# Performance work log

Hardware: AMD Instinct MI355X
Metric: run time of the kernel (lower is better)

Reference implementation:

```python
import jax, jax.numpy as jnp
import numpy as np

B, N, D = 8, 512, 768
HS = 64          # gp_head_size
NT = 12          # len(tag_vocab)
NEG = 1e12


def setup_inputs() -> dict:
    key = jax.random.key(0)
    ks = jax.random.split(key, 14)
    s = 0.02  # init scale for weights
    return {
        "chars": jax.random.normal(ks[0], (B, N, D), dtype=jnp.float32),
        "mask": jax.random.randint(ks[1], (B, N), 0, 2).astype(jnp.int32),
        "w1_ent": jax.random.normal(ks[2], (2 * HS, D), dtype=jnp.float32) * s,
        "b1_ent": jax.random.normal(ks[3], (2 * HS,), dtype=jnp.float32) * s,
        "w2_ent": jax.random.normal(ks[4], (2 * 2, 2 * HS), dtype=jnp.float32) * s,
        "b2_ent": jax.random.normal(ks[5], (2 * 2,), dtype=jnp.float32) * s,
        "w1_head": jax.random.normal(ks[6], (2 * HS, D), dtype=jnp.float32) * s,
        "b1_head": jax.random.normal(ks[7], (2 * HS,), dtype=jnp.float32) * s,
        "w2_head": jax.random.normal(ks[8], (2 * NT, 2 * HS), dtype=jnp.float32) * s,
        "b2_head": jax.random.normal(ks[9], (2 * NT,), dtype=jnp.float32) * s,
        "w1_tail": jax.random.normal(ks[10], (2 * HS, D), dtype=jnp.float32) * s,
        "b1_tail": jax.random.normal(ks[11], (2 * HS,), dtype=jnp.float32) * s,
        "w2_tail": jax.random.normal(ks[12], (2 * NT, 2 * HS), dtype=jnp.float32) * s,
        "b2_tail": jax.random.normal(ks[13], (2 * NT,), dtype=jnp.float32) * s,
    }


def _egp(x, w1, b1, w2, b2, mask, head_size, rope, tril):
    # x: [B,N,D] -> h: [B,N,2*head_size]
    h = jnp.einsum('bnd,ed->bne', x, w1) + b1
    qw, kw = h[..., 0::2], h[..., 1::2]          # [B,N,head_size] each
    if rope:
        n = x.shape[1]
        pos = jnp.arange(n, dtype=x.dtype)
        inv = jnp.power(10000.0, -2.0 * jnp.arange(head_size // 2, dtype=x.dtype) / head_size)
        ang = pos[:, None] * inv[None, :]         # [N, head_size/2]
        cos = jnp.repeat(jnp.cos(ang), 2, axis=-1)[None]  # [1,N,head_size]
        sin = jnp.repeat(jnp.sin(ang), 2, axis=-1)[None]
        def rot(t):
            t2 = jnp.stack([-t[..., 1::2], t[..., 0::2]], axis=-1).reshape(t.shape)
            return t * cos + t2 * sin
        qw, kw = rot(qw), rot(kw)
    logits = jnp.einsum('bmd,bnd->bmn', qw, kw) / (head_size ** 0.5)  # [B,M,N]
    bias = (jnp.einsum('bne,he->bnh', h, w2) + b2).transpose(0, 2, 1) / 2.0  # [B,2H,N]
    # [B,H,M,N]
    logits = logits[:, None] + bias[:, 0::2, None, :] + bias[:, 1::2, :, None]
    m = mask.astype(logits.dtype)
    pad = 1.0 - m[:, None, None, :] * m[:, None, :, None]
    logits = logits - pad * NEG
    if tril:
        tri = jnp.tril(jnp.ones((logits.shape[-2], logits.shape[-1]), logits.dtype), k=-1)
        logits = logits - tri * NEG
    return logits


def reference(chars, mask, w1_ent, b1_ent, w2_ent, b2_ent,
              w1_head, b1_head, w2_head, b2_head,
              w1_tail, b1_tail, w2_tail, b2_tail):
    entity = _egp(chars, w1_ent, b1_ent, w2_ent, b2_ent, mask, HS, True, True)
    head = _egp(chars, w1_head, b1_head, w2_head, b2_head, mask, HS, False, False)
    tail = _egp(chars, w1_tail, b1_tail, w2_tail, b2_tail, mask, HS, False, False)
    return (entity, head, tail)
```

## Files before the change

### kernel.cpp

```cpp
#include <hip/hip_runtime.h>
#include <cstddef>

namespace {
constexpr int B_ = 8;
constexpr int N_ = 512;
constexpr int D_ = 768;
constexpr int HS_ = 64;
constexpr int M_ = B_ * N_;
constexpr int E_ = 2 * HS_;
constexpr float NEGV = 1000000000000.0f;
constexpr float LOG2_10000 = 13.287712379549449f;
}

typedef short mfrag_t __attribute__((ext_vector_type(8)));
typedef float macc_t  __attribute__((ext_vector_type(4)));

__device__ __forceinline__ unsigned short bft(float x) {
    union { float f; unsigned u; } c; c.f = x;
    return (unsigned short)(c.u >> 16);
}

__global__ __launch_bounds__(256) void prep_kernel(
    const float* __restrict__ chars,
    const float* __restrict__ w1e, const float* __restrict__ b1e,
    const float* __restrict__ w2e, const float* __restrict__ b2e,
    const float* __restrict__ w1h, const float* __restrict__ b1h,
    const float* __restrict__ w2h, const float* __restrict__ b2h,
    const float* __restrict__ w1t, const float* __restrict__ b1t,
    const float* __restrict__ w2t, const float* __restrict__ b2t,
    float* __restrict__ h_base,
    float* __restrict__ bias_e, float* __restrict__ bias_h, float* __restrict__ bias_t)
{
    const int fam = blockIdx.y;
    const float* w1 = (fam == 0) ? w1e : (fam == 1) ? w1h : w1t;
    const float* b1 = (fam == 0) ? b1e : (fam == 1) ? b1h : b1t;
    const float* w2 = (fam == 0) ? w2e : (fam == 1) ? w2h : w2t;
    const float* b2 = (fam == 0) ? b2e : (fam == 1) ? b2h : b2t;
    float* bout = (fam == 0) ? bias_e : (fam == 1) ? bias_h : bias_t;
    const int H2 = (fam == 0) ? 4 : 24;
    float* hout = h_base + (size_t)fam * M_ * E_;
    const int m0 = blockIdx.x * 64;

    __shared__ unsigned short A_lds[64][40];
    __shared__ unsigned short B_lds[128][40];
    __shared__ float hs[64][132];

    const int t    = threadIdx.x;
    const int w    = t >> 6;
    const int lane = t & 63;
    const int ml   = lane & 15;
    const int quad = lane >> 4;

    const int ar = t >> 2;
    const int ak = (t & 3) * 8;
    const int bc = t >> 1;
    const int bk = (t & 1) * 16;

    const float* aptr = chars + (size_t)(m0 + ar) * D_ + ak;
    const float* bptr = w1 + (size_t)bc * D_ + bk;

    macc_t acc[8];
    #pragma unroll
    for (int f = 0; f < 8; ++f) acc[f] = (macc_t)0.0f;

    float4 av0 = *(const float4*)(aptr);
    float4 av1 = *(const float4*)(aptr + 4);
    float4 bv0 = *(const float4*)(bptr);
    float4 bv1 = *(const float4*)(bptr + 4);
    float4 bv2 = *(const float4*)(bptr + 8);
    float4 bv3 = *(const float4*)(bptr + 12);

    for (int s = 0; s < 24; ++s) {
        {
            mfrag_t pa;
            pa[0] = (short)bft(av0.x); pa[1] = (short)bft(av0.y);
            pa[2] = (short)bft(av0.z); pa[3] = (short)bft(av0.w);
            pa[4] = (short)bft(av1.x); pa[5] = (short)bft(av1.y);
            pa[6] = (short)bft(av1.z); pa[7] = (short)bft(av1.w);
            *(mfrag_t*)&A_lds[ar][ak] = pa;
            mfrag_t pb0, pb1;
            pb0[0] = (short)bft(bv0.x); pb0[1] = (short)bft(bv0.y);
            pb0[2] = (short)bft(bv0.z); pb0[3] = (short)bft(bv0.w);
            pb0[4] = (short)bft(bv1.x); pb0[5] = (short)bft(bv1.y);
            pb0[6] = (short)bft(bv1.z); pb0[7] = (short)bft(bv1.w);
            pb1[0] = (short)bft(bv2.x); pb1[1] = (short)bft(bv2.y);
            pb1[2] = (short)bft(bv2.z); pb1[3] = (short)bft(bv2.w);
            pb1[4] = (short)bft(bv3.x); pb1[5] = (short)bft(bv3.y);
            pb1[6] = (short)bft(bv3.z); pb1[7] = (short)bft(bv3.w);
            *(mfrag_t*)&B_lds[bc][bk]     = pb0;
            *(mfrag_t*)&B_lds[bc][bk + 8] = pb1;
        }
        __syncthreads();
        if (s < 23) {
            aptr += 32; bptr += 32;
            av0 = *(const float4*)(aptr);
            av1 = *(const float4*)(aptr + 4);
            bv0 = *(const float4*)(bptr);
            bv1 = *(const float4*)(bptr + 4);
            bv2 = *(const float4*)(bptr + 8);
            bv3 = *(const float4*)(bptr + 12);
        }
        const mfrag_t afrag = *(const mfrag_t*)&A_lds[w * 16 + ml][quad * 8];
        #pragma unroll
        for (int f = 0; f < 8; ++f) {
            const mfrag_t bfrag = *(const mfrag_t*)&B_lds[f * 16 + ml][quad * 8];
            acc[f] = __builtin_amdgcn_mfma_f32_16x16x32_bf16(afrag, bfrag, acc[f], 0, 0, 0);
        }
        __syncthreads();
    }

    #pragma unroll
    for (int f = 0; f < 8; ++f) {
        const int col = f * 16 + ml;
        const float bb1 = b1[col];
        #pragma unroll
        for (int r = 0; r < 4; ++r)
            hs[w * 16 + quad * 4 + r][col] = acc[f][r] + bb1;
    }
    __syncthreads();

    {
        const int row = t >> 2;
        const int c0  = (t & 3) * 32;
        float* hp = hout + (size_t)(m0 + row) * E_ + c0;
        #pragma unroll
        for (int q = 0; q < 8; ++q)
            *(float4*)(hp + 4 * q) = *(const float4*)&hs[row][c0 + 4 * q];
    }

    {
        const int row = t & 63;
        const int h2b = t >> 6;
        const int P   = H2 >> 2;
        const int bb  = m0 >> 9;
        const int nb  = (m0 & 511) + row;
        float accv[6] = {0, 0, 0, 0, 0, 0};
        for (int e0 = 0; e0 < E_; e0 += 16) {
            float4 hv0 = *(const float4*)&hs[row][e0];
            float4 hv1 = *(const float4*)&hs[row][e0 + 4];
            float4 hv2 = *(const float4*)&hs[row][e0 + 8];
            float4 hv3 = *(const float4*)&hs[row][e0 + 12];
            for (int p = 0; p < P; ++p) {
                const float* wr = w2 + (size_t)(h2b + 4 * p) * E_ + e0;
                const float4 w0 = *(const float4*)(wr);
                const float4 w1v = *(const float4*)(wr + 4);
                const float4 w2v = *(const float4*)(wr + 8);
                const float4 w3v = *(const float4*)(wr + 12);
                accv[p] += hv0.x * w0.x + hv0.y * w0.y + hv0.z * w0.z + hv0.w * w0.w
                         + hv1.x * w1v.x + hv1.y * w1v.y + hv1.z * w1v.z + hv1.w * w1v.w
                         + hv2.x * w2v.x + hv2.y * w2v.y + hv2.z * w2v.z + hv2.w * w2v.w
                         + hv3.x * w3v.x + hv3.y * w3v.y + hv3.z * w3v.z + hv3.w * w3v.w;
            }
        }
        for (int p = 0; p < P; ++p) {
            const int h2 = h2b + 4 * p;
            bout[((size_t)bb * H2 + h2) * N_ + nb] = (accv[p] + b2[h2]) * 0.5f;
        }
    }
}

template <int H, bool ROPE, bool TRIL>
__device__ __forceinline__ void egp_tile(
    const float* __restrict__ hfam, const float* __restrict__ biasfam,
    const int* __restrict__ mask, float* __restrict__ out,
    int b, int m0, int n0, float (*qtT)[68], float (*kt)[68], int t)
{
    const int srow = t >> 2;
    const int sch  = t & 3;

    {
        const float* hq = hfam + (size_t)(b * N_ + m0 + srow) * E_;
        const float* hk = hfam + (size_t)(b * N_ + n0 + srow) * E_;
        #pragma unroll
        for (int jj = 0; jj < 8; ++jj) {
            const int i = sch + 4 * jj;
            const float4 v = *(const float4*)(hq + 4 * i);
            const float4 w = *(const float4*)(hk + 4 * i);
            if (ROPE) {
                const float inv = exp2f(-(float)i * (LOG2_10000 / 32.0f));
                float sq, cq, sk, ck;
                sincosf((float)(m0 + srow) * inv, &sq, &cq);
                sincosf((float)(n0 + srow) * inv, &sk, &ck);
                qtT[2 * i + 0][srow] = v.x * cq - v.z * sq;
                qtT[2 * i + 1][srow] = v.z * cq + v.x * sq;
                kt [2 * i + 0][srow] = w.y * ck - w.w * sk;
                kt [2 * i + 1][srow] = w.w * ck + w.y * sk;
            } else {
                qtT[2 * i + 0][srow] = v.x;
                qtT[2 * i + 1][srow] = v.z;
                kt [2 * i + 0][srow] = w.y;
                kt [2 * i + 1][srow] = w.w;
            }
        }
    }
    __syncthreads();

    const int rq = t >> 4;
    const int cq = t & 15;

    float acc[4][4] = {};
    #pragma unroll 8
    for (int k = 0; k < 64; ++k) {
        const float4 av = *(const float4*)&qtT[k][4 * rq];
        const float4 kv = *(const float4*)&kt [k][4 * cq];
        acc[0][0] += av.x * kv.x; acc[0][1] += av.x * kv.y; acc[0][2] += av.x * kv.z; acc[0][3] += av.x * kv.w;
        acc[1][0] += av.y * kv.x; acc[1][1] += av.y * kv.y; acc[1][2] += av.y * kv.z; acc[1][3] += av.y * kv.w;
        acc[2][0] += av.z * kv.x; acc[2][1] += av.z * kv.y; acc[2][2] += av.z * kv.z; acc[2][3] += av.z * kv.w;
        acc[3][0] += av.w * kv.x; acc[3][1] += av.w * kv.y; acc[3][2] += av.w * kv.z; acc[3][3] += av.w * kv.w;
    }

    #pragma unroll
    for (int j = 0; j < 4; ++j)
        #pragma unroll
        for (int q = 0; q < 4; ++q) acc[j][q] *= 0.125f;

    int mrow[4], mm[4];
    #pragma unroll
    for (int j = 0; j < 4; ++j) {
        mrow[j] = m0 + 4 * rq + j;
        mm[j]   = mask[b * N_ + mrow[j]];
    }
    const int ncol = n0 + 4 * cq;
    const int4 mnv = *(const int4*)(mask + b * N_ + ncol);
    const int mn[4] = { mnv.x, mnv.y, mnv.z, mnv.w };

    #pragma unroll
    for (int hh = 0; hh < H; ++hh) {
        const float4 be = *(const float4*)(biasfam + ((size_t)b * 2 * H + 2 * hh) * N_ + ncol);
        float bo[4];
        #pragma unroll
        for (int j = 0; j < 4; ++j)
            bo[j] = biasfam[((size_t)b * 2 * H + 2 * hh + 1) * N_ + mrow[j]];

        #pragma unroll
        for (int j = 0; j < 4; ++j) {
            float o[4] = { acc[j][0] + be.x + bo[j], acc[j][1] + be.y + bo[j],
                           acc[j][2] + be.z + bo[j], acc[j][3] + be.w + bo[j] };
            #pragma unroll
            for (int q = 0; q < 4; ++q) {
                if (!(mm[j] & mn[q])) o[q] -= NEGV;
                if (TRIL && (ncol + q) < mrow[j]) o[q] -= NEGV;
            }
            *(float4*)(out + ((size_t)(b * H + hh) * N_ + mrow[j]) * N_ + ncol) =
                make_float4(o[0], o[1], o[2], o[3]);
        }
    }
}

__global__ __launch_bounds__(256) void egp_all_kernel(
    const float* __restrict__ h_base,
    const float* __restrict__ bias_e, const float* __restrict__ bias_h,
    const float* __restrict__ bias_t,
    const int* __restrict__ mask, float* __restrict__ out)
{
    __shared__ float qtT[64][68];
    __shared__ float kt [64][68];

    const int t   = threadIdx.x;
    const int m0  = blockIdx.x * 64;
    const int n0  = blockIdx.y * 64;
    const int fam = blockIdx.z >> 3;
    const int b   = blockIdx.z & 7;

    const size_t ent_sz  = (size_t)B_ * 2 * N_ * N_;
    const size_t head_sz = (size_t)B_ * 12 * N_ * N_;

    if (fam == 0) {
        egp_tile<2, true, true>(h_base, bias_e, mask, out, b, m0, n0, qtT, kt, t);
    } else if (fam == 1) {
        egp_tile<12, false, false>(h_base + (size_t)M_ * E_, bias_h, mask,
                                   out + ent_sz, b, m0, n0, qtT, kt, t);
    } else {
        egp_tile<12, false, false>(h_base + (size_t)2 * M_ * E_, bias_t, mask,
                                   out + ent_sz + head_sz, b, m0, n0, qtT, kt, t);
    }
}

extern "C" void kernel_launch(void* const* d_in, const int* in_sizes, int n_in,
                              void* d_out, int out_size, void* d_ws, size_t ws_size,
                              hipStream_t stream)
{
    const float* chars = (const float*)d_in[0];
    const int*   mask  = (const int*)d_in[1];
    const float* w1e = (const float*)d_in[2];
    const float* b1e = (const float*)d_in[3];
    const float* w2e = (const float*)d_in[4];
    const float* b2e = (const float*)d_in[5];
    const float* w1h = (const float*)d_in[6];
    const float* b1h = (const float*)d_in[7];
    const float* w2h = (const float*)d_in[8];
    const float* b2h = (const float*)d_in[9];
    const float* w1t = (const float*)d_in[10];
    const float* b1t = (const float*)d_in[11];
    const float* w2t = (const float*)d_in[12];
    const float* b2t = (const float*)d_in[13];

    float* out = (float*)d_out;

    float* h_ws   = (float*)d_ws;
    float* bias_e = h_ws + (size_t)3 * M_ * E_;
    float* bias_h = bias_e + (size_t)B_ * 4 * N_;
    float* bias_t = bias_h + (size_t)B_ * 24 * N_;

    prep_kernel<<<dim3(64, 3), 256, 0, stream>>>(
        chars, w1e, b1e, w2e, b2e, w1h, b1h, w2h, b2h, w1t, b1t, w2t, b2t,
        h_ws, bias_e, bias_h, bias_t);

    egp_all_kernel<<<dim3(8, 8, 24), 256, 0, stream>>>(
        h_ws, bias_e, bias_h, bias_t, mask, out);
}
```

Baseline: 297.3 us.

## Precompute RoPE'd bf16 q/k in prep and use MFMA for logits tile

The prep kernel now applies RoPE once per row and writes deinterleaved q and k as bf16 arrays, replacing the fp32 h workspace. The logits kernel reads these directly into MFMA fragments, computes the 64x64 QK^T with bf16 matrix instructions, and stages the result through LDS for the existing bias/mask epilogue. This removes the redundant per-tile sincos, the fp32 scalar FMA loop and the larger h reads. In exchange, q and k are rounded to bf16, which loses precision in the logits. The kernel is likely bound by writing the large fp32 output, which limits the possible gain.

```diff
diff --git a/kernel.cpp b/kernel.cpp
--- a/kernel.cpp
+++ b/kernel.cpp
@@ -19,6 +19,11 @@
     union { float f; unsigned u; } c; c.f = x;
     return (unsigned short)(c.u >> 16);
 }
+__device__ __forceinline__ unsigned short bfrne(float x) {
+    union { float f; unsigned u; } c; c.f = x;
+    const unsigned r = c.u + 0x7FFFu + ((c.u >> 16) & 1u);
+    return (unsigned short)(r >> 16);
+}
 
 __global__ __launch_bounds__(256) void prep_kernel(
     const float* __restrict__ chars,
@@ -28,7 +33,7 @@
     const float* __restrict__ w2h, const float* __restrict__ b2h,
     const float* __restrict__ w1t, const float* __restrict__ b1t,
     const float* __restrict__ w2t, const float* __restrict__ b2t,
-    float* __restrict__ h_base,
+    unsigned short* __restrict__ qbf, unsigned short* __restrict__ kbf,
     float* __restrict__ bias_e, float* __restrict__ bias_h, float* __restrict__ bias_t)
 {
     const int fam = blockIdx.y;
@@ -38,7 +43,8 @@
     const float* b2 = (fam == 0) ? b2e : (fam == 1) ? b2h : b2t;
     float* bout = (fam == 0) ? bias_e : (fam == 1) ? bias_h : bias_t;
     const int H2 = (fam == 0) ? 4 : 24;
-    float* hout = h_base + (size_t)fam * M_ * E_;
+    unsigned short* qout = qbf + (size_t)fam * M_ * HS_;
+    unsigned short* kout = kbf + (size_t)fam * M_ * HS_;
     const int m0 = blockIdx.x * 64;
 
     __shared__ unsigned short A_lds[64][40];
@@ -121,11 +127,37 @@
 
     {
         const int row = t >> 2;
-        const int c0  = (t & 3) * 32;
-        float* hp = hout + (size_t)(m0 + row) * E_ + c0;
-        #pragma unroll
-        for (int q = 0; q < 8; ++q)
-            *(float4*)(hp + 4 * q) = *(const float4*)&hs[row][c0 + 4 * q];
+        const int kg  = t & 3;
+        const float pos = (float)((m0 & 511) + row);
+        unsigned short qv[16], kv[16];
+        #pragma unroll
+        for (int p = 0; p < 8; ++p) {
+            const int i = kg * 8 + p;
+            const float q0 = hs[row][4 * i + 0];
+            const float k0 = hs[row][4 * i + 1];
+            const float q1 = hs[row][4 * i + 2];
+            const float k1 = hs[row][4 * i + 3];
+            if (fam == 0) {
+                const float inv = exp2f(-(float)i * (LOG2_10000 / 32.0f));
+                float sn, cs;
+                sincosf(pos * inv, &sn, &cs);
+                qv[2 * p + 0] = bfrne(q0 * cs - q1 * sn);
+                qv[2 * p + 1] = bfrne(q1 * cs + q0 * sn);
+                kv[2 * p + 0] = bfrne(k0 * cs - k1 * sn);
+                kv[2 * p + 1] = bfrne(k1 * cs + k0 * sn);
+            } else {
+                qv[2 * p + 0] = bfrne(q0);
+                qv[2 * p + 1] = bfrne(q1);
+                kv[2 * p + 0] = bfrne(k0);
+                kv[2 * p + 1] = bfrne(k1);
+            }
+        }
+        unsigned short* qp = qout + (size_t)(m0 + row) * HS_ + kg * 16;
+        unsigned short* kp = kout + (size_t)(m0 + row) * HS_ + kg * 16;
+        *(mfrag_t*)qp       = *(const mfrag_t*)&qv[0];
+        *(mfrag_t*)(qp + 8) = *(const mfrag_t*)&qv[8];
+        *(mfrag_t*)kp       = *(const mfrag_t*)&kv[0];
+        *(mfrag_t*)(kp + 8) = *(const mfrag_t*)&kv[8];
     }
 
     {
@@ -159,60 +191,47 @@
     }
 }
 
-template <int H, bool ROPE, bool TRIL>
+template <int H, bool TRIL>
 __device__ __forceinline__ void egp_tile(
-    const float* __restrict__ hfam, const float* __restrict__ biasfam,
-    const int* __restrict__ mask, float* __restrict__ out,
-    int b, int m0, int n0, float (*qtT)[68], float (*kt)[68], int t)
+    const unsigned short* __restrict__ qf, const unsigned short* __restrict__ kf,
+    const float* __restrict__ biasfam, const int* __restrict__ mask,
+    float* __restrict__ out, int b, int m0, int n0, float (*Cs)[68], int t)
 {
-    const int srow = t >> 2;
-    const int sch  = t & 3;
-
-    {
-        const float* hq = hfam + (size_t)(b * N_ + m0 + srow) * E_;
-        const float* hk = hfam + (size_t)(b * N_ + n0 + srow) * E_;
-        #pragma unroll
-        for (int jj = 0; jj < 8; ++jj) {
-            const int i = sch + 4 * jj;
-            const float4 v = *(const float4*)(hq + 4 * i);
-            const float4 w = *(const float4*)(hk + 4 * i);
-            if (ROPE) {
-                const float inv = exp2f(-(float)i * (LOG2_10000 / 32.0f));
-                float sq, cq, sk, ck;
-                sincosf((float)(m0 + srow) * inv, &sq, &cq);
-                sincosf((float)(n0 + srow) * inv, &sk, &ck);
-                qtT[2 * i + 0][srow] = v.x * cq - v.z * sq;
-                qtT[2 * i + 1][srow] = v.z * cq + v.x * sq;
-                kt [2 * i + 0][srow] = w.y * ck - w.w * sk;
-                kt [2 * i + 1][srow] = w.w * ck + w.y * sk;
-            } else {
-                qtT[2 * i + 0][srow] = v.x;
-                qtT[2 * i + 1][srow] = v.z;
-                kt [2 * i + 0][srow] = w.y;
-                kt [2 * i + 1][srow] = w.w;
-            }
-        }
-    }
+    const int w    = t >> 6;
+    const int lane = t & 63;
+    const int ml   = lane & 15;
+    const int quad = lane >> 4;
+
+    macc_t acc[4];
+    #pragma unroll
+    for (int f = 0; f < 4; ++f) acc[f] = (macc_t)0.0f;
+
+    const unsigned short* qrow = qf + (size_t)(b * N_ + m0 + w * 16 + ml) * HS_ + quad * 8;
+    const unsigned short* krow = kf + (size_t)(b * N_ + n0 + ml) * HS_ + quad * 8;
+
+    #pragma unroll
+    for (int s = 0; s < 2; ++s) {
+        const mfrag_t af = *(const mfrag_t*)(qrow + s * 32);
+        #pragma unroll
+        for (int f = 0; f < 4; ++f) {
+            const mfrag_t bf = *(const mfrag_t*)(krow + (size_t)f * 16 * HS_ + s * 32);
+            acc[f] = __builtin_amdgcn_mfma_f32_16x16x32_bf16(af, bf, acc[f], 0, 0, 0);
+        }
+    }
+
+    #pragma unroll
+    for (int f = 0; f < 4; ++f)
+        #pragma unroll
+        for (int r = 0; r < 4; ++r)
+            Cs[w * 16 + quad * 4 + r][f * 16 + ml] = acc[f][r] * 0.125f;
     __syncthreads();
 
     const int rq = t >> 4;
     const int cq = t & 15;
 
-    float acc[4][4] = {};
-    #pragma unroll 8
-    for (int k = 0; k < 64; ++k) {
-        const float4 av = *(const float4*)&qtT[k][4 * rq];
-        const float4 kv = *(const float4*)&kt [k][4 * cq];
-        acc[0][0] += av.x * kv.x; acc[0][1] += av.x * kv.y; acc[0][2] += av.x * kv.z; acc[0][3] += av.x * kv.w;
-        acc[1][0] += av.y * kv.x; acc[1][1] += av.y * kv.y; acc[1][2] += av.y * kv.z; acc[1][3] += av.y * kv.w;
-        acc[2][0] += av.z * kv.x; acc[2][1] += av.z * kv.y; acc[2][2] += av.z * kv.z; acc[2][3] += av.z * kv.w;
-        acc[3][0] += av.w * kv.x; acc[3][1] += av.w * kv.y; acc[3][2] += av.w * kv.z; acc[3][3] += av.w * kv.w;
-    }
-
-    #pragma unroll
-    for (int j = 0; j < 4; ++j)
-        #pragma unroll
-        for (int q = 0; q < 4; ++q) acc[j][q] *= 0.125f;
+    float4 av[4];
+    #pragma unroll
+    for (int j = 0; j < 4; ++j) av[j] = *(const float4*)&Cs[4 * rq + j][4 * cq];
 
     int mrow[4], mm[4];
     #pragma unroll
@@ -234,8 +253,9 @@
 
         #pragma unroll
         for (int j = 0; j < 4; ++j) {
-            float o[4] = { acc[j][0] + be.x + bo[j], acc[j][1] + be.y + bo[j],
-                           acc[j][2] + be.z + bo[j], acc[j][3] + be.w + bo[j] };
+            const float* aj = (const float*)&av[j];
+            float o[4] = { aj[0] + be.x + bo[j], aj[1] + be.y + bo[j],
+                           aj[2] + be.z + bo[j], aj[3] + be.w + bo[j] };
             #pragma unroll
             for (int q = 0; q < 4; ++q) {
                 if (!(mm[j] & mn[q])) o[q] -= NEGV;
@@ -248,13 +268,12 @@
 }
 
 __global__ __launch_bounds__(256) void egp_all_kernel(
-    const float* __restrict__ h_base,
+    const unsigned short* __restrict__ qbf, const unsigned short* __restrict__ kbf,
     const float* __restrict__ bias_e, const float* __restrict__ bias_h,
     const float* __restrict__ bias_t,
     const int* __restrict__ mask, float* __restrict__ out)
 {
-    __shared__ float qtT[64][68];
-    __shared__ float kt [64][68];
+    __shared__ float Cs[64][68];
 
     const int t   = threadIdx.x;
     const int m0  = blockIdx.x * 64;
@@ -264,15 +283,16 @@
 
     const size_t ent_sz  = (size_t)B_ * 2 * N_ * N_;
     const size_t head_sz = (size_t)B_ * 12 * N_ * N_;
+    const size_t fsl = (size_t)M_ * HS_;
 
     if (fam == 0) {
-        egp_tile<2, true, true>(h_base, bias_e, mask, out, b, m0, n0, qtT, kt, t);
+        egp_tile<2, true>(qbf, kbf, bias_e, mask, out, b, m0, n0, Cs, t);
     } else if (fam == 1) {
-        egp_tile<12, false, false>(h_base + (size_t)M_ * E_, bias_h, mask,
-                                   out + ent_sz, b, m0, n0, qtT, kt, t);
+        egp_tile<12, false>(qbf + fsl, kbf + fsl, bias_h, mask,
+                            out + ent_sz, b, m0, n0, Cs, t);
     } else {
-        egp_tile<12, false, false>(h_base + (size_t)2 * M_ * E_, bias_t, mask,
-                                   out + ent_sz + head_sz, b, m0, n0, qtT, kt, t);
+        egp_tile<12, false>(qbf + 2 * fsl, kbf + 2 * fsl, bias_t, mask,
+                            out + ent_sz + head_sz, b, m0, n0, Cs, t);
     }
 }
 
@@ -297,15 +317,16 @@
 
     float* out = (float*)d_out;
 
-    float* h_ws   = (float*)d_ws;
-    float* bias_e = h_ws + (size_t)3 * M_ * E_;
+    unsigned short* qbf = (unsigned short*)d_ws;
+    unsigned short* kbf = qbf + (size_t)3 * M_ * HS_;
+    float* bias_e = (float*)(kbf + (size_t)3 * M_ * HS_);
     float* bias_h = bias_e + (size_t)B_ * 4 * N_;
     float* bias_t = bias_h + (size_t)B_ * 24 * N_;
 
     prep_kernel<<<dim3(64, 3), 256, 0, stream>>>(
         chars, w1e, b1e, w2e, b2e, w1h, b1h, w2h, b2h, w1t, b1t, w2t, b2t,
-        h_ws, bias_e, bias_h, bias_t);
+        qbf, kbf, bias_e, bias_h, bias_t);
 
     egp_all_kernel<<<dim3(8, 8, 24), 256, 0, stream>>>(
-        h_ws, bias_e, bias_h, bias_t, mask, out);
-}
+        qbf, kbf, bias_e, bias_h, bias_t, mask, out);
+}
```

New measurement: 283.9 us. -4.5%, faster.
